# Kernel optimization log

Hardware: AMD Instinct MI355X
Metric: run time of the kernel (lower is better)

The kernel has to match this reference:

```python
import jax, jax.numpy as jnp
import numpy as np
import math

H = 512
NH = 8
HD = H // NH


def _lin_params(key, out_dim, in_dim):
    k1, k2 = jax.random.split(key)
    bound = 1.0 / math.sqrt(in_dim)
    w = jax.random.uniform(k1, (out_dim, in_dim), minval=-bound, maxval=bound, dtype=jnp.float32)
    b = jax.random.uniform(k2, (out_dim,), minval=-bound, maxval=bound, dtype=jnp.float32)
    return w, b


def setup_inputs() -> dict:
    key = jax.random.key(0)
    ks = jax.random.split(key, 16)
    B, L = 8, 1024
    inp = {
        'hidden_states': jax.random.normal(ks[0], (B, L, H), dtype=jnp.float32),
        'text': jax.random.normal(ks[1], (B, L, H), dtype=jnp.float32),
    }
    names = ['q_img', 'k_img', 'v_img', 'q_txt', 'k_txt', 'v_txt', 'out_img', 'out_txt']
    for i, n in enumerate(names):
        w, b = _lin_params(ks[2 + i], H, H)
        inp['w_' + n] = w
        inp['b_' + n] = b
    wcat, bcat = _lin_params(ks[10], H, 2 * H)
    inp['w_cat'] = wcat
    inp['b_cat'] = bcat
    # nn.MultiheadAttention params: in_proj [3H, H], out_proj [H, H]
    inp['in_proj_w'] = jax.random.normal(ks[11], (3 * H, H), dtype=jnp.float32) * (1.0 / math.sqrt(H))
    inp['in_proj_b'] = jnp.zeros((3 * H,), dtype=jnp.float32)
    pw, pb = _lin_params(ks[12], H, H)
    inp['out_proj_w'] = pw
    inp['out_proj_b'] = pb
    return inp


def _lin(x, w, b):
    return x @ w.T + b


def _heads(x):
    B, L, _ = x.shape
    return x.reshape(B, L, NH, HD).transpose(0, 2, 1, 3)  # [B, NH, L, HD]


def _attn(q, k, v):
    # q,k,v: [B, NH, L, HD]; dropout is identity in eval mode
    scores = jnp.einsum('bhqd,bhkd->bhqk', q, k) / math.sqrt(HD)
    probs = jax.nn.softmax(scores, axis=-1)
    ctx = jnp.einsum('bhqk,bhkd->bhqd', probs, v)
    B, _, L, _ = ctx.shape
    return ctx.transpose(0, 2, 1, 3).reshape(B, L, H)


def reference(hidden_states, text,
              w_q_img, b_q_img, w_k_img, b_k_img, w_v_img, b_v_img,
              w_q_txt, b_q_txt, w_k_txt, b_k_txt, w_v_txt, b_v_txt,
              w_out_img, b_out_img, w_out_txt, b_out_txt,
              w_cat, b_cat, in_proj_w, in_proj_b, out_proj_w, out_proj_b):
    q_img = _heads(_lin(hidden_states, w_q_img, b_q_img))
    k_img = _heads(_lin(hidden_states, w_k_img, b_k_img))
    v_img = _heads(_lin(hidden_states, w_v_img, b_v_img))
    q_txt = _heads(_lin(text, w_q_txt, b_q_txt))
    k_txt = _heads(_lin(text, w_k_txt, b_k_txt))
    v_txt = _heads(_lin(text, w_v_txt, b_v_txt))

    ctx_img = _attn(q_img, k_img, v_img)
    ctx_txt = _attn(q_txt, k_txt, v_txt)
    ctx_it = _attn(q_img, k_txt, v_txt)
    ctx_ti = _attn(q_txt, k_img, v_img)

    out_img = _lin((ctx_img + ctx_it) * 0.5, w_out_img, b_out_img)
    out_txt = _lin((ctx_txt + ctx_ti) * 0.5, w_out_txt, b_out_txt)
    out = _lin(jnp.concatenate([out_img, out_txt], axis=2), w_cat, b_cat)

    # attention pooling (nn.MultiheadAttention self-attention, batch-major math)
    qkv = _lin(out, in_proj_w, in_proj_b)
    q, k, v = jnp.split(qkv, 3, axis=-1)
    ctx = _attn(_heads(q), _heads(k), _heads(v))
    return _lin(ctx, out_proj_w, out_proj_b)
```

## Files before the change

### kernel.cpp

```cpp
#include <hip/hip_runtime.h>

typedef unsigned short u16;
typedef __attribute__((ext_vector_type(4))) unsigned short u16x4;
typedef __attribute__((ext_vector_type(8))) unsigned short u16x8;
typedef __attribute__((ext_vector_type(4))) float f32x4;
typedef __attribute__((ext_vector_type(8))) __bf16 bf16x8;
typedef __attribute__((ext_vector_type(4))) unsigned int u32x4;

#define WS_XH    0UL
#define WS_XT    8388608UL
#define WS_W     16777216UL
#define WS_BQI   24117248UL
#define WS_BQT   24123392UL
#define WS_QKVI  24129536UL
#define WS_QKVT  49295360UL
#define WS_VTI   74461184UL
#define WS_VTT   82849792UL
#define WS_CTXIA 91238400UL
#define WS_CTXTA 99627008UL
#define WS_OCAT  108015616UL
#define WS_OUT2  24129536UL
#define WS_QKVP  32518144UL
#define WS_VTP   57683968UL
#define WS_CTXP  66072576UL

#define SCALE_LOG2E_O8 0.18033688011112042f

__device__ __forceinline__ u16 f2bf(float f) {
  unsigned u = __float_as_uint(f);
  u += 0x7fffu + ((u >> 16) & 1u);
  return (u16)(u >> 16);
}
__device__ __forceinline__ float bf2f(u16 v) {
  return __uint_as_float(((unsigned)v) << 16);
}
__device__ __forceinline__ bf16x8 as_bf(u16x8 v) { return __builtin_bit_cast(bf16x8, v); }
__device__ __forceinline__ f32x4 mfma16(bf16x8 a, bf16x8 b, f32x4 c) {
  return __builtin_amdgcn_mfma_f32_16x16x32_bf16(a, b, c, 0, 0, 0);
}
__device__ __forceinline__ void gload_lds16(const void* g, void* l) {
  __builtin_amdgcn_global_load_lds(
      (const __attribute__((address_space(1))) unsigned int*)g,
      (__attribute__((address_space(3))) unsigned int*)l, 16, 0, 0);
}

__global__ __launch_bounds__(256) void cvt_f32_bf16(const float* __restrict__ s,
                                                    u16* __restrict__ d, int n) {
  int i = (blockIdx.x * 256 + threadIdx.x) * 4;
  if (i >= n) return;
  float4 v = *(const float4*)(s + i);
  u16x4 o;
  o[0] = f2bf(v.x); o[1] = f2bf(v.y); o[2] = f2bf(v.z); o[3] = f2bf(v.w);
  *(u16x4*)(d + i) = o;
}

__global__ __launch_bounds__(256) void prep_weights(
    const float* __restrict__ wqi, const float* __restrict__ wki, const float* __restrict__ wvi,
    const float* __restrict__ wqt, const float* __restrict__ wkt, const float* __restrict__ wvt,
    const float* __restrict__ woi, const float* __restrict__ wot,
    const float* __restrict__ wc,  const float* __restrict__ wip, const float* __restrict__ wop,
    const float* __restrict__ bqi, const float* __restrict__ bki, const float* __restrict__ bvi,
    const float* __restrict__ bqt, const float* __restrict__ bkt, const float* __restrict__ bvt,
    u16* __restrict__ wdst, float* __restrict__ bi, float* __restrict__ bt) {
  int i = blockIdx.x * 256 + threadIdx.x;
  if (i < 786432) {
    const float* s = i < 262144 ? wqi : (i < 524288 ? wki : wvi);
    wdst[i] = f2bf(s[i & 262143]);
  } else if (i < 1572864) {
    int j = i - 786432;
    const float* s = j < 262144 ? wqt : (j < 524288 ? wkt : wvt);
    wdst[i] = f2bf(s[j & 262143]);
  } else if (i < 1835008) wdst[i] = f2bf(woi[i - 1572864]);
  else if (i < 2097152)   wdst[i] = f2bf(wot[i - 1835008]);
  else if (i < 2621440)   wdst[i] = f2bf(wc [i - 2097152]);
  else if (i < 3407872)   wdst[i] = f2bf(wip[i - 2621440]);
  else if (i < 3670016)   wdst[i] = f2bf(wop[i - 3407872]);
  else if (i < 3671552) {
    int j = i - 3670016;
    bi[j] = j < 512 ? bqi[j] : (j < 1024 ? bki[j - 512] : bvi[j - 1024]);
  } else if (i < 3673088) {
    int j = i - 3671552;
    bt[j] = j < 512 ? bqt[j] : (j < 1024 ? bkt[j - 512] : bvt[j - 1024]);
  }
}

__global__ __launch_bounds__(256) void gemm_bf16(
    const u16* __restrict__ A, const u16* __restrict__ A2, int lda,
    const u16* __restrict__ W,
    const float* __restrict__ bias, u16* __restrict__ C, int ldc, int coff, int K,
    int f32out, int qcols, float qscale) {
  __shared__ __align__(16) u16 As[8 * 512];
  __shared__ __align__(16) u16 Bs[8 * 512];
  const int tid = threadIdx.x, lane = tid & 63, wv = tid >> 6;
  const int wm = wv >> 1, wn = wv & 1;
  const int ln15 = lane & 15;
  const int m0 = blockIdx.x * 128, n0 = blockIdx.y * 128;

  const int srow = lane & 15, skc = lane >> 4;
  const u16* gA0 = A + (long)(m0 + wv * 32 + srow) * lda + skc * 8;
  const u16* gW0 = W + (long)(n0 + wv * 32 + srow) * K + skc * 8;
  u16* lA0 = As + (wv * 2) * 512;
  u16* lB0 = Bs + (wv * 2) * 512;

  f32x4 acc[4][4];
#pragma unroll
  for (int j = 0; j < 4; ++j) {
    float bv = bias[n0 + wn * 64 + j * 16 + ln15];
#pragma unroll
    for (int i = 0; i < 4; ++i) acc[i][j] = f32x4{bv, bv, bv, bv};
  }

  for (int k0 = 0; k0 < K; k0 += 32) {
    __syncthreads();
    if (A2 == nullptr) {
      gload_lds16(gA0 + k0, lA0);
      gload_lds16(gA0 + (long)16 * lda + k0, lA0 + 512);
    } else {
#pragma unroll
      for (int blk = 0; blk < 2; ++blk) {
        long gi = (long)(m0 + wv * 32 + blk * 16 + srow) * lda + k0 + skc * 8;
        u16x8 x = *(const u16x8*)(A + gi);
        u16x8 y = *(const u16x8*)(A2 + gi);
        u16x8 r;
#pragma unroll
        for (int u = 0; u < 8; ++u) r[u] = f2bf(bf2f(x[u]) + bf2f(y[u]));
        *(u16x8*)(As + (wv * 2 + blk) * 512 + lane * 8) = r;
      }
    }
    gload_lds16(gW0 + k0, lB0);
    gload_lds16(gW0 + (long)16 * K + k0, lB0 + 512);
    __syncthreads();

    bf16x8 af[4], bfr[4];
#pragma unroll
    for (int i = 0; i < 4; ++i)
      af[i] = as_bf(*(const u16x8*)(As + (wm * 4 + i) * 512 + lane * 8));
#pragma unroll
    for (int j = 0; j < 4; ++j)
      bfr[j] = as_bf(*(const u16x8*)(Bs + (wn * 4 + j) * 512 + lane * 8));
#pragma unroll
    for (int i = 0; i < 4; ++i)
#pragma unroll
      for (int j = 0; j < 4; ++j) acc[i][j] = mfma16(af[i], bfr[j], acc[i][j]);
  }
  const int quad = lane >> 4;
  const int qr4 = quad * 4;
  float colsc[4];
#pragma unroll
  for (int j = 0; j < 4; ++j)
    colsc[j] = (n0 + wn * 64 + j * 16 < qcols) ? qscale : 1.0f;
#pragma unroll
  for (int i = 0; i < 4; ++i)
#pragma unroll
    for (int r = 0; r < 4; ++r) {
      int row = m0 + wm * 64 + i * 16 + qr4 + r;
      long cidx = (long)row * ldc + coff + n0 + wn * 64 + ln15;
      if (f32out) {
        float* cf = (float*)C + cidx;
#pragma unroll
        for (int j = 0; j < 4; ++j) cf[j * 16] = acc[i][j][r] * colsc[j];
      } else {
        u16* cp = C + cidx;
#pragma unroll
        for (int j = 0; j < 4; ++j) cp[j * 16] = f2bf(acc[i][j][r] * colsc[j]);
      }
    }
}

__global__ __launch_bounds__(256) void transpose_v(const u16* __restrict__ src,
                                                   u16* __restrict__ dst) {
  __shared__ __align__(16) u16 T[64][72];
  const int t = threadIdx.x;
  const int l0 = blockIdx.x * 64, h = blockIdx.y, b = blockIdx.z;
  const u16* s = src + (long)b * 1024 * 1536 + 1024 + h * 64;
  {
    int l = t >> 2, co = (t & 3) * 16;
#pragma unroll
    for (int u = 0; u < 2; ++u)
      *(u16x8*)(&T[l][co + u * 8]) = *(const u16x8*)(s + (long)(l0 + l) * 1536 + co + u * 8);
  }
  __syncthreads();
  {
    int d = t >> 2, lo = (t & 3) * 16;
    u16 tmp[16];
#pragma unroll
    for (int u = 0; u < 16; ++u) tmp[u] = T[lo + u][d];
    u16x8 v0, v1;
#pragma unroll
    for (int u = 0; u < 8; ++u) { v0[u] = tmp[u]; v1[u] = tmp[8 + u]; }
    u16* dp = dst + (long)((b * 8 + h) * 64 + d) * 1024 + l0 + lo;
    *(u16x8*)dp = v0;
    *(u16x8*)(dp + 8) = v1;
  }
}

template <int NQF>
__global__ __launch_bounds__(256) void attn_flash(
    const u16* __restrict__ Q, int ldq,
    const u16* __restrict__ KA, const u16* __restrict__ VTA,
    const u16* __restrict__ KB, const u16* __restrict__ VTB, int ldk,
    u16* __restrict__ OA, u16* __restrict__ OB, int ldo, float outscale) {
  __shared__ __align__(16) u16 Kt[32][72];
  __shared__ __align__(16) u16 Vt[64][40];
  __shared__ __align__(16) u16 Pw[4][NQF * 16][56];
  const int tid = threadIdx.x, lane = tid & 63, wv = tid >> 6;
  const int ln15 = lane & 15, quad = lane >> 4, q8 = quad * 8;
  const int h = blockIdx.y, b = blockIdx.z;

  const u16 *K, *VT;
  u16* O;
  int qtile;
  if (KB != nullptr) {
    qtile = blockIdx.x >> 1;
    int phase = blockIdx.x & 1;
    K = phase ? KB : KA;
    VT = phase ? VTB : VTA;
    O = phase ? OB : OA;
  } else {
    qtile = blockIdx.x;
    K = KA; VT = VTA; O = OA;
  }
  const long qrow = (long)b * 1024 + qtile * (NQF * 64) + wv * (NQF * 16);

  bf16x8 qf[NQF][2];
#pragma unroll
  for (int qi = 0; qi < NQF; ++qi) {
    const u16* qp = Q + (qrow + qi * 16 + ln15) * ldq + h * 64;
    qf[qi][0] = as_bf(*(const u16x8*)(qp + q8));
    qf[qi][1] = as_bf(*(const u16x8*)(qp + 32 + q8));
  }

  u16x8 ones_u;
#pragma unroll
  for (int j = 0; j < 8; ++j) ones_u[j] = 0x3F80;
  const bf16x8 onesb = as_bf(ones_u);

  const int kk = tid >> 3, dc = (tid & 7) * 8;
  const int rp = ((kk & 1) << 4) | (kk >> 1);
  const int vd = tid >> 2, ko = (tid & 3) * 8;
  const u16* Kbase = K + ((long)b * 1024 + kk) * ldk + h * 64 + dc;
  const u16* Vbase = VT + ((long)((b * 8 + h) * 64 + vd)) * 1024 + ko;

  f32x4 o[NQF][4];
  f32x4 lacc[NQF];
#pragma unroll
  for (int qi = 0; qi < NQF; ++qi) {
    lacc[qi] = f32x4{0.f, 0.f, 0.f, 0.f};
#pragma unroll
    for (int j = 0; j < 4; ++j) o[qi][j] = f32x4{0.f, 0.f, 0.f, 0.f};
  }

  u32x4 kreg = *(const u32x4*)(Kbase);
  u32x4 vreg = *(const u32x4*)(Vbase);

  for (int k0 = 0; k0 < 1024; k0 += 32) {
    *(u32x4*)(&Kt[rp][dc]) = kreg;
    *(u32x4*)(&Vt[vd][ko]) = vreg;
    __syncthreads();
    if (k0 + 32 < 1024) {
      kreg = *(const u32x4*)(Kbase + (long)(k0 + 32) * ldk);
      vreg = *(const u32x4*)(Vbase + (k0 + 32));
    }

    f32x4 s[2][NQF];
#pragma unroll
    for (int kb = 0; kb < 2; ++kb) {
      bf16x8 b0 = as_bf(*(const u16x8*)(&Kt[kb * 16 + ln15][q8]));
      bf16x8 b1 = as_bf(*(const u16x8*)(&Kt[kb * 16 + ln15][32 + q8]));
#pragma unroll
      for (int qi = 0; qi < NQF; ++qi) {
        f32x4 z = f32x4{0.f, 0.f, 0.f, 0.f};
        z = mfma16(qf[qi][0], b0, z);
        z = mfma16(qf[qi][1], b1, z);
        s[kb][qi] = z;
      }
    }

#pragma unroll
    for (int qi = 0; qi < NQF; ++qi)
#pragma unroll
      for (int r = 0; r < 4; ++r) {
        float p0 = __builtin_amdgcn_exp2f(s[0][qi][r]);
        float p1 = __builtin_amdgcn_exp2f(s[1][qi][r]);
        unsigned u0 = __float_as_uint(p0) + 0x8000u;
        unsigned u1 = __float_as_uint(p1) + 0x8000u;
        unsigned pk = __builtin_amdgcn_perm(u1, u0, 0x07060302);
        *(unsigned*)(&Pw[wv][qi * 16 + quad * 4 + r][2 * ln15]) = pk;
      }
    bf16x8 pa[NQF];
#pragma unroll
    for (int qi = 0; qi < NQF; ++qi) {
      pa[qi] = as_bf(*(const u16x8*)(&Pw[wv][qi * 16 + ln15][q8]));
      lacc[qi] = mfma16(pa[qi], onesb, lacc[qi]);
    }
#pragma unroll
    for (int j = 0; j < 4; ++j) {
      bf16x8 vb = as_bf(*(const u16x8*)(&Vt[j * 16 + ln15][q8]));
#pragma unroll
      for (int qi = 0; qi < NQF; ++qi) o[qi][j] = mfma16(pa[qi], vb, o[qi][j]);
    }
    __syncthreads();
  }

#pragma unroll
  for (int qi = 0; qi < NQF; ++qi)
#pragma unroll
    for (int r = 0; r < 4; ++r) {
      float inv = outscale / lacc[qi][r];
      long row = qrow + qi * 16 + quad * 4 + r;
#pragma unroll
      for (int j = 0; j < 4; ++j)
        O[row * ldo + h * 64 + j * 16 + ln15] = f2bf(o[qi][j][r] * inv);
    }
}

extern "C" void kernel_launch(void* const* d_in, const int* in_sizes, int n_in,
                              void* d_out, int out_size, void* d_ws, size_t ws_size,
                              hipStream_t stream) {
  const float* hidden = (const float*)d_in[0];
  const float* text   = (const float*)d_in[1];
  const float* wqi = (const float*)d_in[2];  const float* bqi = (const float*)d_in[3];
  const float* wki = (const float*)d_in[4];  const float* bki = (const float*)d_in[5];
  const float* wvi = (const float*)d_in[6];  const float* bvi = (const float*)d_in[7];
  const float* wqt = (const float*)d_in[8];  const float* bqt = (const float*)d_in[9];
  const float* wkt = (const float*)d_in[10]; const float* bkt = (const float*)d_in[11];
  const float* wvt = (const float*)d_in[12]; const float* bvt = (const float*)d_in[13];
  const float* woi = (const float*)d_in[14]; const float* boi = (const float*)d_in[15];
  const float* wot = (const float*)d_in[16]; const float* bot = (const float*)d_in[17];
  const float* wc  = (const float*)d_in[18]; const float* bc  = (const float*)d_in[19];
  const float* wip = (const float*)d_in[20]; const float* bip = (const float*)d_in[21];
  const float* wop = (const float*)d_in[22]; const float* bop = (const float*)d_in[23];

  char* ws = (char*)d_ws;
  u16* XH    = (u16*)(ws + WS_XH);
  u16* XT    = (u16*)(ws + WS_XT);
  u16* WB    = (u16*)(ws + WS_W);
  float* BQI = (float*)(ws + WS_BQI);
  float* BQT = (float*)(ws + WS_BQT);
  u16* QKVI  = (u16*)(ws + WS_QKVI);
  u16* QKVT  = (u16*)(ws + WS_QKVT);
  u16* VTI   = (u16*)(ws + WS_VTI);
  u16* VTT   = (u16*)(ws + WS_VTT);
  u16* CTXIA = (u16*)(ws + WS_CTXIA);
  u16* CTXIB = (u16*)(ws + WS_XH);
  u16* CTXTA = (u16*)(ws + WS_CTXTA);
  u16* CTXTB = (u16*)(ws + WS_XT);
  u16* OCAT  = (u16*)(ws + WS_OCAT);
  u16* OUT2  = (u16*)(ws + WS_OUT2);
  u16* QKVP  = (u16*)(ws + WS_QKVP);
  u16* VTP   = (u16*)(ws + WS_VTP);
  u16* CTXP  = (u16*)(ws + WS_CTXP);

  u16* WQKVI = WB;
  u16* WQKVT = WB + 786432;
  u16* WOUTI = WB + 1572864;
  u16* WOUTT = WB + 1835008;
  u16* WCAT  = WB + 2097152;
  u16* WINP  = WB + 2621440;
  u16* WOUTP = WB + 3407872;

  const int NACT = 8192 * 512;

  cvt_f32_bf16<<<dim3(NACT / 1024), 256, 0, stream>>>(hidden, XH, NACT);
  cvt_f32_bf16<<<dim3(NACT / 1024), 256, 0, stream>>>(text, XT, NACT);
  prep_weights<<<dim3(14348), 256, 0, stream>>>(wqi, wki, wvi, wqt, wkt, wvt, woi, wot,
                                                wc, wip, wop, bqi, bki, bvi, bqt, bkt, bvt,
                                                WB, BQI, BQT);
  gemm_bf16<<<dim3(64, 12), 256, 0, stream>>>(XH, nullptr, 512, WQKVI, BQI, QKVI, 1536, 0, 512,
                                              0, 512, SCALE_LOG2E_O8);
  gemm_bf16<<<dim3(64, 12), 256, 0, stream>>>(XT, nullptr, 512, WQKVT, BQT, QKVT, 1536, 0, 512,
                                              0, 512, SCALE_LOG2E_O8);
  transpose_v<<<dim3(16, 8, 8), 256, 0, stream>>>(QKVI, VTI);
  transpose_v<<<dim3(16, 8, 8), 256, 0, stream>>>(QKVT, VTT);
  attn_flash<2><<<dim3(16, 8, 8), 256, 0, stream>>>(QKVI, 1536, QKVI + 512, VTI,
                                                    QKVT + 512, VTT, 1536,
                                                    CTXIA, CTXIB, 512, 0.5f);
  attn_flash<2><<<dim3(16, 8, 8), 256, 0, stream>>>(QKVT, 1536, QKVT + 512, VTT,
                                                    QKVI + 512, VTI, 1536,
                                                    CTXTA, CTXTB, 512, 0.5f);
  gemm_bf16<<<dim3(64, 4), 256, 0, stream>>>(CTXIA, CTXIB, 512, WOUTI, boi, OCAT, 1024, 0, 512,
                                             0, 0, 1.0f);
  gemm_bf16<<<dim3(64, 4), 256, 0, stream>>>(CTXTA, CTXTB, 512, WOUTT, bot, OCAT, 1024, 512, 512,
                                             0, 0, 1.0f);
  gemm_bf16<<<dim3(64, 4), 256, 0, stream>>>(OCAT, nullptr, 1024, WCAT, bc, OUT2, 512, 0, 1024,
                                             0, 0, 1.0f);
  gemm_bf16<<<dim3(64, 12), 256, 0, stream>>>(OUT2, nullptr, 512, WINP, bip, QKVP, 1536, 0, 512,
                                              0, 512, SCALE_LOG2E_O8);
  transpose_v<<<dim3(16, 8, 8), 256, 0, stream>>>(QKVP, VTP);
  attn_flash<1><<<dim3(16, 8, 8), 256, 0, stream>>>(QKVP, 1536, QKVP + 512, VTP,
                                                    nullptr, nullptr, 1536,
                                                    CTXP, nullptr, 512, 1.0f);
  gemm_bf16<<<dim3(64, 4), 256, 0, stream>>>(CTXP, nullptr, 512, WOUTP, bop, (u16*)d_out, 512,
                                             0, 512, 1, 0, 1.0f);
}
```

Measured before the change: 462.7 us.

## Double-buffer GEMM LDS tiles with register prefetch of next K slice

Replaces the direct global-to-LDS loads in the bf16 GEMM with a register-staged, double-buffered pipeline. The next K slice is loaded into registers while the current one is consumed, and only one barrier per iteration remains instead of two. The goal is to hide global load latency and halve synchronisation. In exchange it doubles LDS use and raises register pressure, and it drops the async global_load_lds path.

```diff
diff --git a/kernel.cpp b/kernel.cpp
--- a/kernel.cpp
+++ b/kernel.cpp
@@ -37,11 +37,6 @@
 __device__ __forceinline__ bf16x8 as_bf(u16x8 v) { return __builtin_bit_cast(bf16x8, v); }
 __device__ __forceinline__ f32x4 mfma16(bf16x8 a, bf16x8 b, f32x4 c) {
   return __builtin_amdgcn_mfma_f32_16x16x32_bf16(a, b, c, 0, 0, 0);
-}
-__device__ __forceinline__ void gload_lds16(const void* g, void* l) {
-  __builtin_amdgcn_global_load_lds(
-      (const __attribute__((address_space(1))) unsigned int*)g,
-      (__attribute__((address_space(3))) unsigned int*)l, 16, 0, 0);
 }
 
 __global__ __launch_bounds__(256) void cvt_f32_bf16(const float* __restrict__ s,
@@ -89,8 +84,8 @@
     const u16* __restrict__ W,
     const float* __restrict__ bias, u16* __restrict__ C, int ldc, int coff, int K,
     int f32out, int qcols, float qscale) {
-  __shared__ __align__(16) u16 As[8 * 512];
-  __shared__ __align__(16) u16 Bs[8 * 512];
+  __shared__ __align__(16) u16 As[2][8 * 512];
+  __shared__ __align__(16) u16 Bs[2][8 * 512];
   const int tid = threadIdx.x, lane = tid & 63, wv = tid >> 6;
   const int wm = wv >> 1, wn = wv & 1;
   const int ln15 = lane & 15;
@@ -98,9 +93,11 @@
 
   const int srow = lane & 15, skc = lane >> 4;
   const u16* gA0 = A + (long)(m0 + wv * 32 + srow) * lda + skc * 8;
+  const u16* gA1 = gA0 + (long)16 * lda;
   const u16* gW0 = W + (long)(n0 + wv * 32 + srow) * K + skc * 8;
-  u16* lA0 = As + (wv * 2) * 512;
-  u16* lB0 = Bs + (wv * 2) * 512;
+  const u16* gW1 = gW0 + (long)16 * K;
+  const u16* gA20 = A2 + (long)(m0 + wv * 32 + srow) * lda + skc * 8;
+  const u16* gA21 = gA20 + (long)16 * lda;
 
   f32x4 acc[4][4];
 #pragma unroll
@@ -110,34 +107,45 @@
     for (int i = 0; i < 4; ++i) acc[i][j] = f32x4{bv, bv, bv, bv};
   }
 
-  for (int k0 = 0; k0 < K; k0 += 32) {
+  u16x8 ra0 = *(const u16x8*)(gA0);
+  u16x8 ra1 = *(const u16x8*)(gA1);
+  u16x8 rb0 = *(const u16x8*)(gW0);
+  u16x8 rb1 = *(const u16x8*)(gW1);
+  u16x8 rc0, rc1;
+  if (A2) { rc0 = *(const u16x8*)(gA20); rc1 = *(const u16x8*)(gA21); }
+
+  int buf = 0;
+  for (int k0 = 0; k0 < K; k0 += 32, buf ^= 1) {
+    u16x8 wa0 = ra0, wa1 = ra1;
+    if (A2) {
+#pragma unroll
+      for (int u = 0; u < 8; ++u) {
+        wa0[u] = f2bf(bf2f(ra0[u]) + bf2f(rc0[u]));
+        wa1[u] = f2bf(bf2f(ra1[u]) + bf2f(rc1[u]));
+      }
+    }
+    u16* la = As[buf] + (wv * 2) * 512;
+    u16* lb = Bs[buf] + (wv * 2) * 512;
+    *(u16x8*)(la + lane * 8) = wa0;
+    *(u16x8*)(la + 512 + lane * 8) = wa1;
+    *(u16x8*)(lb + lane * 8) = rb0;
+    *(u16x8*)(lb + 512 + lane * 8) = rb1;
+    if (k0 + 32 < K) {
+      ra0 = *(const u16x8*)(gA0 + k0 + 32);
+      ra1 = *(const u16x8*)(gA1 + k0 + 32);
+      rb0 = *(const u16x8*)(gW0 + k0 + 32);
+      rb1 = *(const u16x8*)(gW1 + k0 + 32);
+      if (A2) { rc0 = *(const u16x8*)(gA20 + k0 + 32); rc1 = *(const u16x8*)(gA21 + k0 + 32); }
+    }
     __syncthreads();
-    if (A2 == nullptr) {
-      gload_lds16(gA0 + k0, lA0);
-      gload_lds16(gA0 + (long)16 * lda + k0, lA0 + 512);
-    } else {
-#pragma unroll
-      for (int blk = 0; blk < 2; ++blk) {
-        long gi = (long)(m0 + wv * 32 + blk * 16 + srow) * lda + k0 + skc * 8;
-        u16x8 x = *(const u16x8*)(A + gi);
-        u16x8 y = *(const u16x8*)(A2 + gi);
-        u16x8 r;
-#pragma unroll
-        for (int u = 0; u < 8; ++u) r[u] = f2bf(bf2f(x[u]) + bf2f(y[u]));
-        *(u16x8*)(As + (wv * 2 + blk) * 512 + lane * 8) = r;
-      }
-    }
-    gload_lds16(gW0 + k0, lB0);
-    gload_lds16(gW0 + (long)16 * K + k0, lB0 + 512);
-    __syncthreads();
 
     bf16x8 af[4], bfr[4];
 #pragma unroll
     for (int i = 0; i < 4; ++i)
-      af[i] = as_bf(*(const u16x8*)(As + (wm * 4 + i) * 512 + lane * 8));
+      af[i] = as_bf(*(const u16x8*)(As[buf] + (wm * 4 + i) * 512 + lane * 8));
 #pragma unroll
     for (int j = 0; j < 4; ++j)
-      bfr[j] = as_bf(*(const u16x8*)(Bs + (wn * 4 + j) * 512 + lane * 8));
+      bfr[j] = as_bf(*(const u16x8*)(Bs[buf] + (wn * 4 + j) * 512 + lane * 8));
 #pragma unroll
     for (int i = 0; i < 4; ++i)
 #pragma unroll
```

Result: faster. 436.6 us (-5.6%).
